# Kernel optimization log

Hardware: AMD Instinct MI355X
Metric: run time of the kernel (lower is better)

## Reference

```python
import jax, jax.numpy as jnp
import numpy as np

N_QUAT = 4
VERONESE_DIM = 10
OUT_FEATURES = 132

# static index sets matching torch.triu_indices(4, 4)
_rows, _cols = np.triu_indices(N_QUAT)          # 10 upper-tri entries
_mask = _rows != _cols
TRIU_ROWS = jnp.asarray(_rows)
TRIU_COLS = jnp.asarray(_cols)
SYM_ROWS = jnp.asarray(_cols[_mask])            # mirrored lower-tri
SYM_COLS = jnp.asarray(_rows[_mask])
SYM_Z_IDX = jnp.asarray(np.nonzero(_mask)[0])


def setup_inputs() -> dict:
    key = jax.random.key(0)
    k_z, k_w1, k_w2 = jax.random.split(key, 3)
    B, D_IN, D_HID, D_OUT_NN = 65536, 256, 1024, 128
    z = jax.random.normal(k_z, (B, D_IN), dtype=jnp.float32)
    W1 = jax.random.normal(k_w1, (D_IN, D_HID), dtype=jnp.float32) * 0.02
    b1 = jnp.zeros((D_HID,), dtype=jnp.float32)
    W2 = jax.random.normal(k_w2, (D_HID, D_OUT_NN), dtype=jnp.float32) * 0.02
    b2 = jnp.zeros((D_OUT_NN,), dtype=jnp.float32)
    return {"z": z, "W1": W1, "b1": b1, "W2": W2, "b2": b2}


def _recover_quat(z_v):
    # z_v: (B, 10) -> symmetric (B, 4, 4) -> top eigenvector -> (B, 4)
    B = z_v.shape[0]
    M = jnp.zeros((B, N_QUAT, N_QUAT), dtype=z_v.dtype)
    M = M.at[:, TRIU_ROWS, TRIU_COLS].set(z_v)
    M = M.at[:, SYM_ROWS, SYM_COLS].set(z_v[:, SYM_Z_IDX])
    _, vecs = jnp.linalg.eigh(M)          # eigenvalues ascending
    q = vecs[:, :, -1]                    # eigenvector of largest eigenvalue
    sign = jnp.sign(q[:, 0:1] + 1e-9)
    return q * sign


def reference(z, W1, b1, W2, b2):
    orig_shape = z.shape
    zf = z.reshape(-1, orig_shape[-1])           # (B, in_features)
    q_pred = _recover_quat(zf[:, :VERONESE_DIM])  # (B, 4)
    h = jax.nn.relu(zf @ W1 + b1)
    others = h @ W2 + b2                          # (B, 128)
    B = zf.shape[0]
    out = jnp.zeros((B, OUT_FEATURES), dtype=zf.dtype)
    out = out.at[:, :N_QUAT].set(q_pred)          # quat_indices = [0,1,2,3]
    out = out.at[:, N_QUAT:].set(others)          # non_quat = [4..131]
    return out.reshape(*orig_shape[:-1], OUT_FEATURES)
```

## Files before the change

kernel.cpp:

```cpp
#include <hip/hip_runtime.h>


typedef short s16x8 __attribute__((ext_vector_type(8)));
typedef float f32x4 __attribute__((ext_vector_type(4)));
typedef unsigned char u8;

__device__ __forceinline__ f32x4 mfma16(s16x8 a, s16x8 b, f32x4 c) {
    return __builtin_amdgcn_mfma_f32_16x16x32_bf16(a, b, c, 0, 0, 0);
}

__device__ __forceinline__ short f2bf(float f) {
    unsigned int u = __float_as_uint(f);
    u = (u + 0x7fffu + ((u >> 16) & 1u)) >> 16;
    return (short)u;
}

__device__ __forceinline__ void gload_lds16(const void* g, void* l) {
    __builtin_amdgcn_global_load_lds(
        (const __attribute__((address_space(1))) unsigned int*)g,
        (__attribute__((address_space(3))) unsigned int*)l, 16, 0, 0);
}

__global__ __launch_bounds__(256) void prep_weights(
    const float* __restrict__ W1, const float* __restrict__ W2,
    uint4* __restrict__ w1t, uint4* __restrict__ w2t)
{
    int tid = blockIdx.x * 256 + threadIdx.x;
    union { short b[8]; uint4 v; } pk;
    if (tid < 32768) {
        int u  = tid >> 10;
        int n1 = tid & 1023;
        #pragma unroll
        for (int j = 0; j < 8; ++j)
            pk.b[j] = f2bf(W1[(u * 8 + j) * 1024 + n1]);
        w1t[n1 * 32 + (u ^ (n1 & 7))] = pk.v;
    } else {
        int id = tid - 32768;
        int U  = id >> 7;
        int n2 = id & 127;
        #pragma unroll
        for (int j = 0; j < 8; ++j)
            pk.b[j] = f2bf(W2[(U * 8 + j) * 128 + n2]);
        w2t[n2 * 128 + (U ^ (n2 & 7))] = pk.v;
    }
}

__global__ __launch_bounds__(512, 2) void fused_all(
    const float* __restrict__ z, const float* __restrict__ b1,
    const float* __restrict__ b2, const uint4* __restrict__ w1t,
    const uint4* __restrict__ w2t, float* __restrict__ out)
{
    __shared__ __align__(16) u8 lds[135168];
    u8* const bs1 = lds;
    u8* const bs2 = lds + 65536;
    u8* const hsb = lds + 98304;
    u8* const bls = lds + 131072;

    const int t    = threadIdx.x;
    const int lane = t & 63;
    const int w    = t >> 6;
    const int q    = lane >> 4;
    const int r16  = lane & 15;
    const int bm0  = blockIdx.x * 256;
    const int rowbase = bm0 + w * 32;
    u8* const hw = hsb + w * 4096;

    #pragma unroll
    for (int i = 0; i < 4; ++i) { int f = i * 512 + t; gload_lds16(w1t + f, bs1 + f * 16); }
    #pragma unroll
    for (int i = 0; i < 2; ++i) { int f = i * 512 + t; gload_lds16(w2t + (f >> 3) * 128 + (f & 7), bs2 + f * 16); }
    if (w < 4) gload_lds16(b1 + t * 4, bls + t * 16);

    if (lane < 32) {
        int row = rowbase + lane;
        const float* zr = z + (size_t)row * 256;
        float4 v0 = *(const float4*)(zr);
        float4 v1 = *(const float4*)(zr + 4);
        float2 v2 = *(const float2*)(zr + 8);

        float A[4][4] = {{v0.x, v0.y, v0.z, v0.w},
                         {v0.y, v1.x, v1.y, v1.z},
                         {v0.z, v1.y, v1.w, v2.x},
                         {v0.w, v1.z, v2.x, v2.y}};
        float V[4][4] = {{1.f, 0.f, 0.f, 0.f},
                         {0.f, 1.f, 0.f, 0.f},
                         {0.f, 0.f, 1.f, 0.f},
                         {0.f, 0.f, 0.f, 1.f}};

#define ROT(p, qq) do {                                                   \
        float apq  = A[p][qq];                                            \
        float tau  = (A[qq][qq] - A[p][p]) *                              \
                     __builtin_amdgcn_rcpf(2.0f * apq);                   \
        float tt   = __builtin_amdgcn_rcpf(                               \
                        fabsf(tau) +                                      \
                        __builtin_amdgcn_sqrtf(fmaf(tau, tau, 1.0f)));    \
        tt = copysignf(tt, tau);                                          \
        tt = (fabsf(apq) > 1e-20f) ? tt : 0.0f;                           \
        float cth = __builtin_amdgcn_rsqf(fmaf(tt, tt, 1.0f));            \
        float sth = tt * cth;                                             \
        _Pragma("unroll")                                                 \
        for (int k = 0; k < 4; ++k) {                                     \
            float akp = A[k][p], akq = A[k][qq];                          \
            A[k][p]  = cth * akp - sth * akq;                             \
            A[k][qq] = sth * akp + cth * akq;                             \
        }                                                                 \
        _Pragma("unroll")                                                 \
        for (int k = 0; k < 4; ++k) {                                     \
            float apk = A[p][k], aqk = A[qq][k];                          \
            A[p][k]  = cth * apk - sth * aqk;                             \
            A[qq][k] = sth * apk + cth * aqk;                             \
        }                                                                 \
        _Pragma("unroll")                                                 \
        for (int k = 0; k < 4; ++k) {                                     \
            float vkp = V[k][p], vkq = V[k][qq];                          \
            V[k][p]  = cth * vkp - sth * vkq;                             \
            V[k][qq] = sth * vkp + cth * vkq;                             \
        }                                                                 \
    } while (0)

        #pragma unroll 1
        for (int sweep = 0; sweep < 8; ++sweep) {
            ROT(0, 1); ROT(0, 2); ROT(0, 3); ROT(1, 2); ROT(1, 3); ROT(2, 3);
        }
#undef ROT

        float bv = A[0][0];
        float q0 = V[0][0], q1 = V[1][0], q2 = V[2][0], q3 = V[3][0];
        #pragma unroll
        for (int k = 1; k < 4; ++k) {
            bool better = A[k][k] > bv;
            bv = better ? A[k][k] : bv;
            q0 = better ? V[0][k] : q0;
            q1 = better ? V[1][k] : q1;
            q2 = better ? V[2][k] : q2;
            q3 = better ? V[3][k] : q3;
        }
        float sgn = (q0 + 1e-9f) >= 0.0f ? 1.0f : -1.0f;
        *(float4*)(out + (size_t)row * 132) =
            make_float4(sgn * q0, sgn * q1, sgn * q2, sgn * q3);
    }

    const f32x4 zero4 = {0.f, 0.f, 0.f, 0.f};
    s16x8 zf[2][8];
    #pragma unroll
    for (int mr = 0; mr < 2; ++mr) {
        const float* zp = z + (size_t)(rowbase + mr * 16 + r16) * 256;
        #pragma unroll
        for (int s = 0; s < 8; ++s) {
            const float4* p = (const float4*)(zp + s * 32 + q * 8);
            float4 a0 = p[0], a1 = p[1];
            s16x8 a;
            a[0] = f2bf(a0.x); a[1] = f2bf(a0.y); a[2] = f2bf(a0.z); a[3] = f2bf(a0.w);
            a[4] = f2bf(a1.x); a[5] = f2bf(a1.y); a[6] = f2bf(a1.z); a[7] = f2bf(a1.w);
            zf[mr][s] = a;
        }
    }

    f32x4 acc2[2][8];
    #pragma unroll
    for (int mr = 0; mr < 2; ++mr)
        #pragma unroll
        for (int n = 0; n < 8; ++n) acc2[mr][n] = zero4;

    __syncthreads();

    const int e      = r16 & 7;
    const int qx16   = (q ^ (e & 3)) << 4;
    const int e464   = (e & 4) << 4;
    const int base512 = r16 * 512 + qx16 + e464;
    const int base128 = r16 * 128 + qx16 + e464;
    const int e2     = (r16 >> 1) & 3;
    const int whb    = r16 * 128 + (((q >> 1) ^ (r16 & 1)) << 4) + (q & 1) * 8;

    auto chunk = [&](int c, int B1, int B2) {
        if (c < 15) {
            const uint4* s1 = w1t + (c + 1) * 2048;
            const int B1n = B1 ^ 32768, B2n = B2 ^ 16384;
            #pragma unroll
            for (int i = 0; i < 4; ++i) {
                int f = i * 512 + t;
                gload_lds16(s1 + f, bs1 + B1n + f * 16);
            }
            #pragma unroll
            for (int i = 0; i < 2; ++i) {
                int f = i * 512 + t;
                gload_lds16(w2t + (f >> 3) * 128 + (c + 1) * 8 + (f & 7),
                            bs2 + B2n + f * 16);
            }
        }

        const u8* a0p = bs1 + B1 + base512;
        const u8* a1p = bs1 + B1 + (base512 ^ 64);
        const u8* bb  = bls + c * 256 + q * 16;

        #pragma unroll
        for (int ct = 0; ct < 4; ++ct) {
            f32x4 a0 = zero4, a1 = zero4;
            #pragma unroll
            for (int s = 0; s < 8; ++s) {
                const u8* ap = (s & 1) ? a1p : a0p;
                s16x8 afr = *(const s16x8*)(ap + ct * 8192 + (s >> 1) * 128);
                a0 = mfma16(afr, zf[0][s], a0);
                a1 = mfma16(afr, zf[1][s], a1);
            }
            f32x4 bv = *(const f32x4*)(bb + ct * 64);
            const int wo = whb + ((ct ^ e2) << 5);
            #pragma unroll
            for (int mr = 0; mr < 2; ++mr) {
                f32x4 av = mr ? a1 : a0;
                union { short h[4]; unsigned long long v; } pk;
                pk.h[0] = f2bf(fmaxf(av[0] + bv[0], 0.f));
                pk.h[1] = f2bf(fmaxf(av[1] + bv[1], 0.f));
                pk.h[2] = f2bf(fmaxf(av[2] + bv[2], 0.f));
                pk.h[3] = f2bf(fmaxf(av[3] + bv[3], 0.f));
                *(unsigned long long*)(hw + wo + mr * 2048) = pk.v;
            }
        }

        #pragma unroll
        for (int s2 = 0; s2 < 2; ++s2) {
            const int boff = s2 ? (base128 ^ 64) : base128;
            const u8* hr = hw + boff;
            const u8* br = bs2 + B2 + boff;
            s16x8 af0 = *(const s16x8*)(hr);
            s16x8 af1 = *(const s16x8*)(hr + 2048);
            #pragma unroll
            for (int ct2 = 0; ct2 < 8; ++ct2) {
                s16x8 bfr = *(const s16x8*)(br + ct2 * 2048);
                acc2[0][ct2] = mfma16(af0, bfr, acc2[0][ct2]);
                acc2[1][ct2] = mfma16(af1, bfr, acc2[1][ct2]);
            }
        }

        __syncthreads();
    };

    #pragma unroll 1
    for (int cc = 0; cc < 8; ++cc) {
        chunk(2 * cc,     0,     0);
        chunk(2 * cc + 1, 32768, 16384);
    }

    #pragma unroll
    for (int ct2 = 0; ct2 < 8; ++ct2) {
        const float b2v = b2[ct2 * 16 + r16];
        #pragma unroll
        for (int mr = 0; mr < 2; ++mr) {
            #pragma unroll
            for (int r = 0; r < 4; ++r) {
                int m = w * 32 + mr * 16 + q * 4 + r;
                out[(size_t)(bm0 + m) * 132 + 4 + ct2 * 16 + r16] =
                    acc2[mr][ct2][r] + b2v;
            }
        }
    }
}

extern "C" void kernel_launch(void* const* d_in, const int* in_sizes, int n_in,
                              void* d_out, int out_size, void* d_ws, size_t ws_size,
                              hipStream_t stream) {
    const float* z  = (const float*)d_in[0];
    const float* W1 = (const float*)d_in[1];
    const float* b1 = (const float*)d_in[2];
    const float* W2 = (const float*)d_in[3];
    const float* b2 = (const float*)d_in[4];
    float* out = (float*)d_out;

    uint4* w1t = (uint4*)d_ws;
    uint4* w2t = (uint4*)((char*)d_ws + 512 * 1024);

    hipLaunchKernelGGL(prep_weights, dim3(192), dim3(256), 0, stream,
                       W1, W2, w1t, w2t);
    hipLaunchKernelGGL(fused_all, dim3(256), dim3(512), 0, stream,
                       z, b1, b2, (const uint4*)w1t, (const uint4*)w2t, out);
}
```

Baseline: 75.44 us.

## Pre-pack weights in fragment order, use packed bf16 converts, fewer Jacobi sweeps

The weight prep kernel now writes W1 and W2 in exact MFMA fragment order, so each lane reads a contiguous 16-byte fragment at lane*16 without XOR swizzle arithmetic. The global-to-LDS copies become linear, and the hidden-activation layout is rearranged to match. Float-to-bf16 conversion now uses the hardware v_cvt_pk_bf16_f32 instruction instead of manual rounding. The Jacobi eigen-solve drops from 8 to 6 sweeps, which saves work but risks a less converged quaternion on hard matrices.

```diff
diff --git a/kernel.cpp b/kernel.cpp
--- a/kernel.cpp
+++ b/kernel.cpp
@@ -13,6 +13,12 @@
     unsigned int u = __float_as_uint(f);
     u = (u + 0x7fffu + ((u >> 16) & 1u)) >> 16;
     return (short)u;
+}
+
+__device__ __forceinline__ unsigned cvt_pk(float lo, float hi) {
+    unsigned r;
+    asm("v_cvt_pk_bf16_f32 %0, %1, %2" : "=v"(r) : "v"(lo), "v"(hi));
+    return r;
 }
 
 __device__ __forceinline__ void gload_lds16(const void* g, void* l) {
@@ -26,22 +32,29 @@
     uint4* __restrict__ w1t, uint4* __restrict__ w2t)
 {
     int tid = blockIdx.x * 256 + threadIdx.x;
+    int q = (tid >> 4) & 3, r16 = tid & 15;
     union { short b[8]; uint4 v; } pk;
     if (tid < 32768) {
-        int u  = tid >> 10;
-        int n1 = tid & 1023;
+        int s  = (tid >> 6) & 7;
+        int ct = (tid >> 9) & 3;
+        int c  = tid >> 11;
+        int k0 = s * 32 + q * 8;
+        int n1 = c * 64 + ct * 16 + r16;
         #pragma unroll
         for (int j = 0; j < 8; ++j)
-            pk.b[j] = f2bf(W1[(u * 8 + j) * 1024 + n1]);
-        w1t[n1 * 32 + (u ^ (n1 & 7))] = pk.v;
+            pk.b[j] = f2bf(W1[(k0 + j) * 1024 + n1]);
+        w1t[tid] = pk.v;
     } else {
-        int id = tid - 32768;
-        int U  = id >> 7;
-        int n2 = id & 127;
+        int f   = tid - 32768;
+        int ct2 = (f >> 6) & 7;
+        int s2  = (f >> 9) & 1;
+        int c   = f >> 10;
+        int k0  = c * 64 + s2 * 32 + q * 8;
+        int n2  = ct2 * 16 + r16;
         #pragma unroll
         for (int j = 0; j < 8; ++j)
-            pk.b[j] = f2bf(W2[(U * 8 + j) * 128 + n2]);
-        w2t[n2 * 128 + (U ^ (n2 & 7))] = pk.v;
+            pk.b[j] = f2bf(W2[(k0 + j) * 128 + n2]);
+        w2t[f] = pk.v;
     }
 }
 
@@ -51,10 +64,6 @@
     const uint4* __restrict__ w2t, float* __restrict__ out)
 {
     __shared__ __align__(16) u8 lds[135168];
-    u8* const bs1 = lds;
-    u8* const bs2 = lds + 65536;
-    u8* const hsb = lds + 98304;
-    u8* const bls = lds + 131072;
 
     const int t    = threadIdx.x;
     const int lane = t & 63;
@@ -63,13 +72,18 @@
     const int r16  = lane & 15;
     const int bm0  = blockIdx.x * 256;
     const int rowbase = bm0 + w * 32;
-    u8* const hw = hsb + w * 4096;
-
-    #pragma unroll
-    for (int i = 0; i < 4; ++i) { int f = i * 512 + t; gload_lds16(w1t + f, bs1 + f * 16); }
-    #pragma unroll
-    for (int i = 0; i < 2; ++i) { int f = i * 512 + t; gload_lds16(w2t + (f >> 3) * 128 + (f & 7), bs2 + f * 16); }
-    if (w < 4) gload_lds16(b1 + t * 4, bls + t * 16);
+
+    #pragma unroll
+    for (int i = 0; i < 4; ++i) {
+        int f = i * 512 + t;
+        gload_lds16(w1t + f, lds + f * 16);
+    }
+    #pragma unroll
+    for (int i = 0; i < 2; ++i) {
+        int f = i * 512 + t;
+        gload_lds16(w2t + f, lds + 65536 + f * 16);
+    }
+    if (t < 256) gload_lds16(b1 + t * 4, lds + 131072 + t * 16);
 
     if (lane < 32) {
         int row = rowbase + lane;
@@ -119,7 +133,7 @@
     } while (0)
 
         #pragma unroll 1
-        for (int sweep = 0; sweep < 8; ++sweep) {
+        for (int sweep = 0; sweep < 6; ++sweep) {
             ROT(0, 1); ROT(0, 2); ROT(0, 3); ROT(1, 2); ROT(1, 3); ROT(2, 3);
         }
 #undef ROT
@@ -144,15 +158,17 @@
     s16x8 zf[2][8];
     #pragma unroll
     for (int mr = 0; mr < 2; ++mr) {
-        const float* zp = z + (size_t)(rowbase + mr * 16 + r16) * 256;
+        const float* zp = z + (size_t)(rowbase + mr * 16 + r16) * 256 + q * 8;
         #pragma unroll
         for (int s = 0; s < 8; ++s) {
-            const float4* p = (const float4*)(zp + s * 32 + q * 8);
+            const float4* p = (const float4*)(zp + s * 32);
             float4 a0 = p[0], a1 = p[1];
-            s16x8 a;
-            a[0] = f2bf(a0.x); a[1] = f2bf(a0.y); a[2] = f2bf(a0.z); a[3] = f2bf(a0.w);
-            a[4] = f2bf(a1.x); a[5] = f2bf(a1.y); a[6] = f2bf(a1.z); a[7] = f2bf(a1.w);
-            zf[mr][s] = a;
+            union { unsigned u[4]; s16x8 v; } pk;
+            pk.u[0] = cvt_pk(a0.x, a0.y);
+            pk.u[1] = cvt_pk(a0.z, a0.w);
+            pk.u[2] = cvt_pk(a1.x, a1.y);
+            pk.u[3] = cvt_pk(a1.z, a1.w);
+            zf[mr][s] = pk.v;
         }
     }
 
@@ -164,69 +180,61 @@
 
     __syncthreads();
 
-    const int e      = r16 & 7;
-    const int qx16   = (q ^ (e & 3)) << 4;
-    const int e464   = (e & 4) << 4;
-    const int base512 = r16 * 512 + qx16 + e464;
-    const int base128 = r16 * 128 + qx16 + e464;
-    const int e2     = (r16 >> 1) & 3;
-    const int whb    = r16 * 128 + (((q >> 1) ^ (r16 & 1)) << 4) + (q & 1) * 8;
-
-    auto chunk = [&](int c, int B1, int B2) {
+    const u8* const aW0 = lds + lane * 16;
+    const u8* const aW1 = lds + 32768 + lane * 16;
+    const u8* const bW0 = lds + 65536 + lane * 16;
+    const u8* const bW1 = lds + 81920 + lane * 16;
+    u8* const hwv       = lds + 98304 + w * 4096;
+    const u8* const hr  = hwv + lane * 16;
+    u8* const hwr = hwv + r16 * 16 + (q >> 1) * 256 + (q & 1) * 8;
+    const u8* const blsp = lds + 131072 + q * 16;
+
+    auto chunk = [&](int c, const u8* a, const u8* bW,
+                     u8* s1dst, u8* s2dst) {
         if (c < 15) {
             const uint4* s1 = w1t + (c + 1) * 2048;
-            const int B1n = B1 ^ 32768, B2n = B2 ^ 16384;
+            const uint4* s2 = w2t + (c + 1) * 1024;
             #pragma unroll
             for (int i = 0; i < 4; ++i) {
                 int f = i * 512 + t;
-                gload_lds16(s1 + f, bs1 + B1n + f * 16);
+                gload_lds16(s1 + f, s1dst + f * 16);
             }
             #pragma unroll
             for (int i = 0; i < 2; ++i) {
                 int f = i * 512 + t;
-                gload_lds16(w2t + (f >> 3) * 128 + (c + 1) * 8 + (f & 7),
-                            bs2 + B2n + f * 16);
-            }
-        }
-
-        const u8* a0p = bs1 + B1 + base512;
-        const u8* a1p = bs1 + B1 + (base512 ^ 64);
-        const u8* bb  = bls + c * 256 + q * 16;
+                gload_lds16(s2 + f, s2dst + f * 16);
+            }
+        }
 
         #pragma unroll
         for (int ct = 0; ct < 4; ++ct) {
             f32x4 a0 = zero4, a1 = zero4;
             #pragma unroll
             for (int s = 0; s < 8; ++s) {
-                const u8* ap = (s & 1) ? a1p : a0p;
-                s16x8 afr = *(const s16x8*)(ap + ct * 8192 + (s >> 1) * 128);
+                s16x8 afr = *(const s16x8*)(a + (ct * 8 + s) * 1024);
                 a0 = mfma16(afr, zf[0][s], a0);
                 a1 = mfma16(afr, zf[1][s], a1);
             }
-            f32x4 bv = *(const f32x4*)(bb + ct * 64);
-            const int wo = whb + ((ct ^ e2) << 5);
+            f32x4 bv = *(const f32x4*)(blsp + c * 256 + ct * 64);
             #pragma unroll
             for (int mr = 0; mr < 2; ++mr) {
                 f32x4 av = mr ? a1 : a0;
-                union { short h[4]; unsigned long long v; } pk;
-                pk.h[0] = f2bf(fmaxf(av[0] + bv[0], 0.f));
-                pk.h[1] = f2bf(fmaxf(av[1] + bv[1], 0.f));
-                pk.h[2] = f2bf(fmaxf(av[2] + bv[2], 0.f));
-                pk.h[3] = f2bf(fmaxf(av[3] + bv[3], 0.f));
-                *(unsigned long long*)(hw + wo + mr * 2048) = pk.v;
+                uint2 hp;
+                hp.x = cvt_pk(fmaxf(av[0] + bv[0], 0.f),
+                              fmaxf(av[1] + bv[1], 0.f));
+                hp.y = cvt_pk(fmaxf(av[2] + bv[2], 0.f),
+                              fmaxf(av[3] + bv[3], 0.f));
+                *(uint2*)(hwr + mr * 2048 + ct * 512) = hp;
             }
         }
 
         #pragma unroll
         for (int s2 = 0; s2 < 2; ++s2) {
-            const int boff = s2 ? (base128 ^ 64) : base128;
-            const u8* hr = hw + boff;
-            const u8* br = bs2 + B2 + boff;
-            s16x8 af0 = *(const s16x8*)(hr);
-            s16x8 af1 = *(const s16x8*)(hr + 2048);
+            s16x8 af0 = *(const s16x8*)(hr + s2 * 1024);
+            s16x8 af1 = *(const s16x8*)(hr + 2048 + s2 * 1024);
             #pragma unroll
             for (int ct2 = 0; ct2 < 8; ++ct2) {
-                s16x8 bfr = *(const s16x8*)(br + ct2 * 2048);
+                s16x8 bfr = *(const s16x8*)(bW + (s2 * 8 + ct2) * 1024);
                 acc2[0][ct2] = mfma16(af0, bfr, acc2[0][ct2]);
                 acc2[1][ct2] = mfma16(af1, bfr, acc2[1][ct2]);
             }
@@ -235,10 +243,15 @@
         __syncthreads();
     };
 
+    u8* const s1b0 = lds;
+    u8* const s1b1 = lds + 32768;
+    u8* const s2b0 = lds + 65536;
+    u8* const s2b1 = lds + 81920;
+
     #pragma unroll 1
     for (int cc = 0; cc < 8; ++cc) {
-        chunk(2 * cc,     0,     0);
-        chunk(2 * cc + 1, 32768, 16384);
+        chunk(2 * cc,     aW0, bW0, s1b1, s2b1);
+        chunk(2 * cc + 1, aW1, bW1, s1b0, s2b0);
     }
 
     #pragma unroll
```

Result: faster. 67.25 us (-10.9%).
